# Optimization experiments

Measured on AMD Instinct MI355X. Metric: run time of the kernel, lower is better.

## Reference

```python
import jax, jax.numpy as jnp
import numpy as np

N_NODES = 100000
N_EDGES = 3200000
IN_CH = 128
OUT_CH = 64
HID = 2 * OUT_CH  # 128


def gcn_conv(x, W, b, src, dst, num_nodes):
    """PyG GCNConv: D^{-1/2}(A+I)D^{-1/2} X W + b (add_self_loops=True, normalize=True)."""
    h = x @ W  # [N, C_out]
    # degree on target nodes, edge weight 1, plus 1 for the self loop
    deg = jax.ops.segment_sum(jnp.ones_like(dst, dtype=h.dtype), dst, num_segments=num_nodes) + 1.0
    dinv = jax.lax.rsqrt(deg)  # deg >= 1 so no inf handling needed
    norm = dinv[src] * dinv[dst]  # [E]
    agg = jax.ops.segment_sum(h[src] * norm[:, None], dst, num_segments=num_nodes)
    agg = agg + h * (dinv * dinv)[:, None]  # self-loop contribution, norm = dinv_i^2
    return agg + b


def setup_inputs() -> dict:
    key = jax.random.key(0)
    ks = jax.random.split(key, 8)
    s_in = 1.0 / np.sqrt(IN_CH)
    s_hid = 1.0 / np.sqrt(HID)
    s_out = 1.0 / np.sqrt(OUT_CH)
    return {
        "x": jax.random.normal(ks[0], (N_NODES, IN_CH), dtype=jnp.float32),
        "edge_index": jax.random.randint(ks[1], (2, N_EDGES), 0, N_NODES, dtype=jnp.int64),
        "W1n": jax.random.normal(ks[2], (IN_CH, HID), dtype=jnp.float32) * s_in,
        "b1n": jnp.zeros((HID,), jnp.float32),
        "W2n": jax.random.normal(ks[3], (HID, OUT_CH), dtype=jnp.float32) * s_hid,
        "b2n": jnp.zeros((OUT_CH,), jnp.float32),
        "W1e": jax.random.normal(ks[4], (OUT_CH, HID), dtype=jnp.float32) * s_out,
        "b1e": jnp.zeros((HID,), jnp.float32),
        "W2e": jax.random.normal(ks[5], (HID, OUT_CH), dtype=jnp.float32) * s_hid,
        "b2e": jnp.zeros((OUT_CH,), jnp.float32),
    }


def reference(x, edge_index, W1n, b1n, W2n, b2n, W1e, b1e, W2e, b2e):
    src, dst = edge_index[0], edge_index[1]
    n = x.shape[0]
    h = jax.nn.relu(gcn_conv(x, W1n, b1n, src, dst, n))
    mu = gcn_conv(h, W2n, b2n, src, dst, n)
    e = jax.nn.relu(gcn_conv(mu, W1e, b1e, src, dst, n))
    logstd = gcn_conv(e, W2e, b2e, src, dst, n)
    return (mu, logstd)
```

## Files before the change

kernel.cpp:

```cpp
#include <hip/hip_runtime.h>
#include <hip/hip_bf16.h>


typedef unsigned int uint;
typedef unsigned short ushort_t;
typedef __attribute__((ext_vector_type(8))) short bf16x8;
typedef __attribute__((ext_vector_type(4))) float f32x4;

__device__ __forceinline__ float bflo(uint u) { return __uint_as_float(u << 16); }
__device__ __forceinline__ float bfhi(uint u) { return __uint_as_float(u & 0xFFFF0000u); }
__device__ __forceinline__ ushort_t f2bf(float f) {
  union { float f; uint u; } v; v.f = f;
  uint r = v.u + 0x7FFFu + ((v.u >> 16) & 1u);
  return (ushort_t)(r >> 16);
}

#define BSH 4
#define SCAP 128
#define BFCAP 1024


__global__ void k_scatter(const int* __restrict__ src, const int* __restrict__ dst,
                          int E, int* __restrict__ cnt, uint* __restrict__ ebuf) {
  int i = blockIdx.x * 256 + threadIdx.x;
  const int sub = blockIdx.x & 7;
  if (2 * i + 1 < E) {
    int2 s2 = *(const int2*)(src + 2 * i);
    int2 d2 = *(const int2*)(dst + 2 * i);
    int c0 = ((d2.x >> BSH) << 3) + sub;
    int p0 = atomicAdd(&cnt[c0], 1);
    if (p0 < SCAP) ebuf[c0 * SCAP + p0] = (uint)s2.x | ((uint)(d2.x & 15) << 17);
    int c1 = ((d2.y >> BSH) << 3) + sub;
    int p1 = atomicAdd(&cnt[c1], 1);
    if (p1 < SCAP) ebuf[c1 * SCAP + p1] = (uint)s2.y | ((uint)(d2.y & 15) << 17);
  }
}

__global__ __launch_bounds__(1024) void k_bscan(const int* __restrict__ cnt,
                                                int* __restrict__ boffs,
                                                int NBK, int E) {
  __shared__ int sc[1024];
  const int t = threadIdx.x;
  int run = 0;
  for (int base = 0; base < NBK; base += 1024) {
    int i = base + t;
    int c = 0;
    if (i < NBK) {
      const int4* q = (const int4*)(cnt + i * 8);
      int4 a = q[0], b = q[1];
      c = a.x + a.y + a.z + a.w + b.x + b.y + b.z + b.w;
    }
    sc[t] = c;
    __syncthreads();
    for (int off = 1; off < 1024; off <<= 1) {
      int u = (t >= off) ? sc[t - off] : 0;
      __syncthreads();
      sc[t] += u;
      __syncthreads();
    }
    if (i < NBK) boffs[i] = run + sc[t] - c;
    int total = sc[1023];
    __syncthreads();
    run += total;
  }
  if (t == 0) boffs[NBK] = E;
}

__global__ __launch_bounds__(256) void k_binfill(const int* __restrict__ cnt,
                                                 const int* __restrict__ boffs,
                                                 const uint* __restrict__ ebuf,
                                                 int* __restrict__ csr,
                                                 int* __restrict__ offs,
                                                 float* __restrict__ dinv,
                                                 int N, int E) {
  __shared__ uint led[BFCAP];
  __shared__ int lcnt[16], lbase[16], lpre[9];
  const int b = blockIdx.x;
  const int t = threadIdx.x;
  if (t < 16) lcnt[t] = 0;
  if (t == 0) {
    int r = 0;
#pragma unroll
    for (int s = 0; s < 8; s++) {
      lpre[s] = r;
      int c = cnt[b * 8 + s];
      r += (c < SCAP ? c : SCAP);
    }
    lpre[8] = r;
  }
  __syncthreads();
#pragma unroll
  for (int s = 0; s < 8; s++) {
    int base = lpre[s], len = lpre[s + 1] - base;
    for (int e = t; e < len; e += 256) led[base + e] = ebuf[(b * 8 + s) * SCAP + e];
  }
  const int total = lpre[8];
  __syncthreads();
  for (int e = t; e < total; e += 256) atomicAdd(&lcnt[(led[e] >> 17) & 15], 1);
  __syncthreads();
  if (t == 0) {
    int run = boffs[b];
#pragma unroll
    for (int k = 0; k < 16; k++) { lbase[k] = run; run += lcnt[k]; }
  }
  __syncthreads();
  if (t < 16) {
    int node = (b << BSH) + t;
    if (node < N) {
      offs[node] = lbase[t];
      dinv[node] = rsqrtf((float)(lcnt[t] + 1));
    }
  }
  if (b == 0 && t == 16) offs[N] = E;
  if (t < 16) lcnt[t] = 0;
  __syncthreads();
  for (int e = t; e < total; e += 256) {
    uint p = led[e];
    int k = (int)((p >> 17) & 15);
    int r = atomicAdd(&lcnt[k], 1);
    csr[lbase[k] + r] = (int)(p & 0x1FFFF);
  }
}


__global__ void k_cvt(const float* __restrict__ in, uint* __restrict__ out, int n8) {
  int i = blockIdx.x * 256 + threadIdx.x;
  if (i < n8) {
    float4 a = *(const float4*)(in + 8 * i);
    float4 b = *(const float4*)(in + 8 * i + 4);
    uint4 o;
    o.x = (uint)f2bf(a.x) | ((uint)f2bf(a.y) << 16);
    o.y = (uint)f2bf(a.z) | ((uint)f2bf(a.w) << 16);
    o.z = (uint)f2bf(b.x) | ((uint)f2bf(b.y) << 16);
    o.w = (uint)f2bf(b.z) | ((uint)f2bf(b.w) << 16);
    *(uint4*)(out + 4 * i) = o;
  }
}


template <int CIN, int COUT>
__global__ __launch_bounds__(256) void k_mgemm(const __hip_bfloat16* __restrict__ X,
                                               const float* __restrict__ W,
                                               const float* __restrict__ dinv,
                                               __hip_bfloat16* __restrict__ H, int N) {
  constexpr int KCH = CIN / 32;
  constexpr int TPW = COUT / 64;
  const int wid = threadIdx.x >> 6, lane = threadIdx.x & 63;
  const int l16 = lane & 15, lg = lane >> 4;
  const int cb = wid * (COUT / 4);
  bf16x8 bfr[TPW][KCH];
#pragma unroll
  for (int t = 0; t < TPW; t++) {
#pragma unroll
    for (int ch = 0; ch < KCH; ch++) {
      const int col = cb + t * 16 + l16;
      const int k0 = ch * 32 + lg * 8;
#pragma unroll
      for (int j = 0; j < 8; j++)
        bfr[t][ch][j] = (short)f2bf(W[(size_t)(k0 + j) * COUT + col]);
    }
  }
  const int RB = (N + 15) >> 4;
  for (int rb = blockIdx.x; rb < RB; rb += gridDim.x) {
    const int r0 = rb << 4;
    const int arow = min(r0 + l16, N - 1);
    const __hip_bfloat16* xr = X + (size_t)arow * CIN + lg * 8;
    bf16x8 afr[KCH];
#pragma unroll
    for (int ch = 0; ch < KCH; ch++) afr[ch] = *(const bf16x8*)(xr + ch * 32);
    f32x4 acc[TPW];
#pragma unroll
    for (int t = 0; t < TPW; t++) acc[t] = (f32x4){0.f, 0.f, 0.f, 0.f};
#pragma unroll
    for (int ch = 0; ch < KCH; ch++) {
#pragma unroll
      for (int t = 0; t < TPW; t++)
        acc[t] = __builtin_amdgcn_mfma_f32_16x16x32_bf16(afr[ch], bfr[t][ch], acc[t], 0, 0, 0);
    }
#pragma unroll
    for (int r = 0; r < 4; r++) {
      const int orow = r0 + lg * 4 + r;
      if (orow < N) {
        const float dv = dinv[orow];
#pragma unroll
        for (int t = 0; t < TPW; t++)
          *(ushort_t*)(H + (size_t)orow * COUT + cb + t * 16 + l16) = f2bf(dv * acc[t][r]);
      }
    }
  }
}


__global__ __launch_bounds__(256) void k_agg128(const __hip_bfloat16* __restrict__ H,
                                                const int* __restrict__ offs,
                                                const int* __restrict__ csr,
                                                const float* __restrict__ dinv,
                                                const float* __restrict__ b,
                                                __hip_bfloat16* __restrict__ OUT, int N) {
  const int lane = threadIdx.x & 63, wid = threadIdx.x >> 6;
  const int i = blockIdx.x * 4 + wid;
  if (i >= N) return;
  const int c = lane * 2;
  const float b0 = b[c], b1 = b[c + 1];
  const int beg = offs[i], end = offs[i + 1];
  float a0 = 0, a1 = 0;
  int e = beg;
  for (; e + 4 <= end; e += 4) {
    int s0 = csr[e], s1 = csr[e + 1], s2 = csr[e + 2], s3 = csr[e + 3];
    uint h0 = *(const uint*)(H + (size_t)s0 * 128 + c);
    uint h1 = *(const uint*)(H + (size_t)s1 * 128 + c);
    uint h2 = *(const uint*)(H + (size_t)s2 * 128 + c);
    uint h3 = *(const uint*)(H + (size_t)s3 * 128 + c);
    a0 += bflo(h0) + bflo(h1) + bflo(h2) + bflo(h3);
    a1 += bfhi(h0) + bfhi(h1) + bfhi(h2) + bfhi(h3);
  }
  for (; e < end; e++) {
    int s = csr[e];
    uint h = *(const uint*)(H + (size_t)s * 128 + c);
    a0 += bflo(h);
    a1 += bfhi(h);
  }
  const float di = dinv[i];
  uint hs = *(const uint*)(H + (size_t)i * 128 + c);
  float r0 = di * (a0 + bflo(hs)) + b0;
  float r1 = di * (a1 + bfhi(hs)) + b1;
  r0 = fmaxf(r0, 0.f);
  r1 = fmaxf(r1, 0.f);
  *(uint*)(OUT + (size_t)i * 128 + c) = (uint)f2bf(r0) | ((uint)f2bf(r1) << 16);
}


__global__ __launch_bounds__(256) void k_agg64(const __hip_bfloat16* __restrict__ H,
                                               const int* __restrict__ offs,
                                               const int* __restrict__ csr,
                                               const float* __restrict__ dinv,
                                               const float* __restrict__ b,
                                               float* __restrict__ OUT,
                                               __hip_bfloat16* __restrict__ MIR, int N) {
  const int lane = threadIdx.x & 63, wid = threadIdx.x >> 6;
  const int i = blockIdx.x * 4 + wid;
  if (i >= N) return;
  const int half = lane >> 5;
  const int c = (lane & 31) * 2;
  const float b0 = b[c], b1 = b[c + 1];
  const int beg = offs[i], end = offs[i + 1];
  float a0 = 0, a1 = 0;
  int e = beg + half;
  for (; e + 6 < end; e += 8) {
    int s0 = csr[e], s1 = csr[e + 2], s2 = csr[e + 4], s3 = csr[e + 6];
    uint h0 = *(const uint*)(H + (size_t)s0 * 64 + c);
    uint h1 = *(const uint*)(H + (size_t)s1 * 64 + c);
    uint h2 = *(const uint*)(H + (size_t)s2 * 64 + c);
    uint h3 = *(const uint*)(H + (size_t)s3 * 64 + c);
    a0 += bflo(h0) + bflo(h1) + bflo(h2) + bflo(h3);
    a1 += bfhi(h0) + bfhi(h1) + bfhi(h2) + bfhi(h3);
  }
  for (; e < end; e += 2) {
    int s = csr[e];
    uint h = *(const uint*)(H + (size_t)s * 64 + c);
    a0 += bflo(h);
    a1 += bfhi(h);
  }
  a0 += __shfl_xor(a0, 32);
  a1 += __shfl_xor(a1, 32);
  const float di = dinv[i];
  uint hs = *(const uint*)(H + (size_t)i * 64 + c);
  float r0 = di * (a0 + bflo(hs)) + b0;
  float r1 = di * (a1 + bfhi(hs)) + b1;
  if (lane < 32) {
    *(float2*)(OUT + (size_t)i * 64 + c) = make_float2(r0, r1);
    if (MIR) *(uint*)(MIR + (size_t)i * 64 + c) = (uint)f2bf(r0) | ((uint)f2bf(r1) << 16);
  }
}


extern "C" void kernel_launch(void* const* d_in, const int* in_sizes, int n_in,
                              void* d_out, int out_size, void* d_ws, size_t ws_size,
                              hipStream_t stream) {
  const float* x   = (const float*)d_in[0];
  const int*   ei  = (const int*)d_in[1];
  const float* W1n = (const float*)d_in[2];
  const float* b1n = (const float*)d_in[3];
  const float* W2n = (const float*)d_in[4];
  const float* b2n = (const float*)d_in[5];
  const float* W1e = (const float*)d_in[6];
  const float* b1e = (const float*)d_in[7];
  const float* W2e = (const float*)d_in[8];
  const float* b2e = (const float*)d_in[9];
  float* out = (float*)d_out;

  const int N = in_sizes[0] / 128;
  const int E = in_sizes[1] / 2;
  const int NBK = (N + 15) >> BSH;
  const int* src = ei;
  const int* dst = ei + E;

  char* p = (char*)d_ws;
  auto alloc = [&](size_t bytes) {
    void* q = (void*)p;
    p += (bytes + 255) & ~(size_t)255;
    return q;
  };
  int*   cnt   = (int*)alloc((size_t)NBK * 8 * 4);
  int*   boffs = (int*)alloc((size_t)(NBK + 1) * 4);
  int*   offs  = (int*)alloc((size_t)(N + 1) * 4);
  float* dinv  = (float*)alloc((size_t)N * 4);
  int*   csr   = (int*)alloc((size_t)E * 4);
  __hip_bfloat16* hbuf = (__hip_bfloat16*)alloc((size_t)N * 128 * 2);
  __hip_bfloat16* abuf = (__hip_bfloat16*)alloc((size_t)N * 128 * 2);
  uint* ebuf = (uint*)hbuf;

  const int RB = (N + 15) >> 4;
  const int GEMM_GRID = RB < 1024 ? RB : 1024;

  hipMemsetAsync(cnt, 0, (size_t)NBK * 8 * 4, stream);
  k_scatter<<<(E / 2 + 255) / 256, 256, 0, stream>>>(src, dst, E, cnt, ebuf);
  k_bscan<<<1, 1024, 0, stream>>>(cnt, boffs, NBK, E);
  k_binfill<<<NBK, 256, 0, stream>>>(cnt, boffs, ebuf, csr, offs, dinv, N, E);

  k_cvt<<<(N * 128 / 8 + 255) / 256, 256, 0, stream>>>(x, (uint*)abuf, N * 128 / 8);

  k_mgemm<128, 128><<<GEMM_GRID, 256, 0, stream>>>(abuf, W1n, dinv, hbuf, N);
  k_agg128<<<(N + 3) / 4, 256, 0, stream>>>(hbuf, offs, csr, dinv, b1n, abuf, N);

  k_mgemm<128, 64><<<GEMM_GRID, 256, 0, stream>>>(abuf, W2n, dinv, hbuf, N);
  k_agg64<<<(N + 3) / 4, 256, 0, stream>>>(hbuf, offs, csr, dinv, b2n, out, abuf, N);

  k_mgemm<64, 128><<<GEMM_GRID, 256, 0, stream>>>(abuf, W1e, dinv, hbuf, N);
  k_agg128<<<(N + 3) / 4, 256, 0, stream>>>(hbuf, offs, csr, dinv, b1e, abuf, N);

  k_mgemm<128, 64><<<GEMM_GRID, 256, 0, stream>>>(abuf, W2e, dinv, hbuf, N);
  k_agg64<<<(N + 3) / 4, 256, 0, stream>>>(hbuf, offs, csr, dinv, b2e, out + (size_t)N * 64,
                                           (__hip_bfloat16*)nullptr, N);
}
```

Before: 766.6 us.

## Slice aggregation by 16-column feature chunks with persistent grid; XCC-based scatter sub-bucket

The aggregation kernels now run on a fixed persistent grid. Each wave processes a 16-column slice of the feature matrix for every node before moving to the next slice, with 8 edges handled in parallel per wave and shuffle reductions. The goal is to shrink the gather working set per pass (32 B per row) so that the randomly accessed H slice fits in cache across the edge gather. The cost is 8 or 4 passes over the CSR indices and narrow 4-byte gathers. The scatter kernel also picks its sub-bucket from the hardware XCC id register instead of the block index, which lowers cross-die atomic contention.

After: 1.573 ms. +105.2%, slower.

```diff
diff --git a/kernel.cpp b/kernel.cpp
--- a/kernel.cpp
+++ b/kernel.cpp
@@ -18,12 +18,15 @@
 #define BSH 4
 #define SCAP 128
 #define BFCAP 1024
+#define AGG_GRID 2048
+
+#define XCC_HWREG 6164
 
 
 __global__ void k_scatter(const int* __restrict__ src, const int* __restrict__ dst,
                           int E, int* __restrict__ cnt, uint* __restrict__ ebuf) {
   int i = blockIdx.x * 256 + threadIdx.x;
-  const int sub = blockIdx.x & 7;
+  const int sub = __builtin_amdgcn_s_getreg(XCC_HWREG) & 7;
   if (2 * i + 1 < E) {
     int2 s2 = *(const int2*)(src + 2 * i);
     int2 d2 = *(const int2*)(dst + 2 * i);
@@ -197,38 +200,48 @@
                                                 const float* __restrict__ dinv,
                                                 const float* __restrict__ b,
                                                 __hip_bfloat16* __restrict__ OUT, int N) {
-  const int lane = threadIdx.x & 63, wid = threadIdx.x >> 6;
-  const int i = blockIdx.x * 4 + wid;
-  if (i >= N) return;
-  const int c = lane * 2;
-  const float b0 = b[c], b1 = b[c + 1];
-  const int beg = offs[i], end = offs[i + 1];
-  float a0 = 0, a1 = 0;
-  int e = beg;
-  for (; e + 4 <= end; e += 4) {
-    int s0 = csr[e], s1 = csr[e + 1], s2 = csr[e + 2], s3 = csr[e + 3];
-    uint h0 = *(const uint*)(H + (size_t)s0 * 128 + c);
-    uint h1 = *(const uint*)(H + (size_t)s1 * 128 + c);
-    uint h2 = *(const uint*)(H + (size_t)s2 * 128 + c);
-    uint h3 = *(const uint*)(H + (size_t)s3 * 128 + c);
-    a0 += bflo(h0) + bflo(h1) + bflo(h2) + bflo(h3);
-    a1 += bfhi(h0) + bfhi(h1) + bfhi(h2) + bfhi(h3);
-  }
-  for (; e < end; e++) {
-    int s = csr[e];
-    uint h = *(const uint*)(H + (size_t)s * 128 + c);
-    a0 += bflo(h);
-    a1 += bfhi(h);
-  }
-  const float di = dinv[i];
-  uint hs = *(const uint*)(H + (size_t)i * 128 + c);
-  float r0 = di * (a0 + bflo(hs)) + b0;
-  float r1 = di * (a1 + bfhi(hs)) + b1;
-  r0 = fmaxf(r0, 0.f);
-  r1 = fmaxf(r1, 0.f);
-  *(uint*)(OUT + (size_t)i * 128 + c) = (uint)f2bf(r0) | ((uint)f2bf(r1) << 16);
-}
-
+  const int lane = threadIdx.x & 63;
+  const int gw = (blockIdx.x * 256 + threadIdx.x) >> 6;
+  const int TW = AGG_GRID * 4;
+  const int ep = lane >> 3;
+  const int c = (lane & 7) * 2;
+#pragma unroll 1
+  for (int s = 0; s < 8; s++) {
+    const int cbase = s * 16 + c;
+    const float b0 = b[cbase], b1 = b[cbase + 1];
+    const __hip_bfloat16* Hs = H + cbase;
+    for (int i = gw; i < N; i += TW) {
+      const int beg = offs[i], end = offs[i + 1];
+      float a0 = 0, a1 = 0;
+      int e = beg + ep;
+      for (; e + 8 < end; e += 16) {
+        int s0 = csr[e], s1 = csr[e + 8];
+        uint h0 = *(const uint*)(Hs + (size_t)s0 * 128);
+        uint h1 = *(const uint*)(Hs + (size_t)s1 * 128);
+        a0 += bflo(h0) + bflo(h1);
+        a1 += bfhi(h0) + bfhi(h1);
+      }
+      if (e < end) {
+        int s0 = csr[e];
+        uint h0 = *(const uint*)(Hs + (size_t)s0 * 128);
+        a0 += bflo(h0);
+        a1 += bfhi(h0);
+      }
+      a0 += __shfl_xor(a0, 8);  a1 += __shfl_xor(a1, 8);
+      a0 += __shfl_xor(a0, 16); a1 += __shfl_xor(a1, 16);
+      a0 += __shfl_xor(a0, 32); a1 += __shfl_xor(a1, 32);
+      if (ep == 0) {
+        const float di = dinv[i];
+        uint hs = *(const uint*)(Hs + (size_t)i * 128);
+        float r0 = di * (a0 + bflo(hs)) + b0;
+        float r1 = di * (a1 + bfhi(hs)) + b1;
+        r0 = fmaxf(r0, 0.f);
+        r1 = fmaxf(r1, 0.f);
+        *(uint*)(OUT + (size_t)i * 128 + cbase) = (uint)f2bf(r0) | ((uint)f2bf(r1) << 16);
+      }
+    }
+  }
+}
 
 __global__ __launch_bounds__(256) void k_agg64(const __hip_bfloat16* __restrict__ H,
                                                const int* __restrict__ offs,
@@ -237,39 +250,45 @@
                                                const float* __restrict__ b,
                                                float* __restrict__ OUT,
                                                __hip_bfloat16* __restrict__ MIR, int N) {
-  const int lane = threadIdx.x & 63, wid = threadIdx.x >> 6;
-  const int i = blockIdx.x * 4 + wid;
-  if (i >= N) return;
-  const int half = lane >> 5;
-  const int c = (lane & 31) * 2;
-  const float b0 = b[c], b1 = b[c + 1];
-  const int beg = offs[i], end = offs[i + 1];
-  float a0 = 0, a1 = 0;
-  int e = beg + half;
-  for (; e + 6 < end; e += 8) {
-    int s0 = csr[e], s1 = csr[e + 2], s2 = csr[e + 4], s3 = csr[e + 6];
-    uint h0 = *(const uint*)(H + (size_t)s0 * 64 + c);
-    uint h1 = *(const uint*)(H + (size_t)s1 * 64 + c);
-    uint h2 = *(const uint*)(H + (size_t)s2 * 64 + c);
-    uint h3 = *(const uint*)(H + (size_t)s3 * 64 + c);
-    a0 += bflo(h0) + bflo(h1) + bflo(h2) + bflo(h3);
-    a1 += bfhi(h0) + bfhi(h1) + bfhi(h2) + bfhi(h3);
-  }
-  for (; e < end; e += 2) {
-    int s = csr[e];
-    uint h = *(const uint*)(H + (size_t)s * 64 + c);
-    a0 += bflo(h);
-    a1 += bfhi(h);
-  }
-  a0 += __shfl_xor(a0, 32);
-  a1 += __shfl_xor(a1, 32);
-  const float di = dinv[i];
-  uint hs = *(const uint*)(H + (size_t)i * 64 + c);
-  float r0 = di * (a0 + bflo(hs)) + b0;
-  float r1 = di * (a1 + bfhi(hs)) + b1;
-  if (lane < 32) {
-    *(float2*)(OUT + (size_t)i * 64 + c) = make_float2(r0, r1);
-    if (MIR) *(uint*)(MIR + (size_t)i * 64 + c) = (uint)f2bf(r0) | ((uint)f2bf(r1) << 16);
+  const int lane = threadIdx.x & 63;
+  const int gw = (blockIdx.x * 256 + threadIdx.x) >> 6;
+  const int TW = AGG_GRID * 4;
+  const int ep = lane >> 3;
+  const int c = (lane & 7) * 2;
+#pragma unroll 1
+  for (int s = 0; s < 4; s++) {
+    const int cbase = s * 16 + c;
+    const float b0 = b[cbase], b1 = b[cbase + 1];
+    const __hip_bfloat16* Hs = H + cbase;
+    for (int i = gw; i < N; i += TW) {
+      const int beg = offs[i], end = offs[i + 1];
+      float a0 = 0, a1 = 0;
+      int e = beg + ep;
+      for (; e + 8 < end; e += 16) {
+        int s0 = csr[e], s1 = csr[e + 8];
+        uint h0 = *(const uint*)(Hs + (size_t)s0 * 64);
+        uint h1 = *(const uint*)(Hs + (size_t)s1 * 64);
+        a0 += bflo(h0) + bflo(h1);
+        a1 += bfhi(h0) + bfhi(h1);
+      }
+      if (e < end) {
+        int s0 = csr[e];
+        uint h0 = *(const uint*)(Hs + (size_t)s0 * 64);
+        a0 += bflo(h0);
+        a1 += bfhi(h0);
+      }
+      a0 += __shfl_xor(a0, 8);  a1 += __shfl_xor(a1, 8);
+      a0 += __shfl_xor(a0, 16); a1 += __shfl_xor(a1, 16);
+      a0 += __shfl_xor(a0, 32); a1 += __shfl_xor(a1, 32);
+      if (ep == 0) {
+        const float di = dinv[i];
+        uint hs = *(const uint*)(Hs + (size_t)i * 64);
+        float r0 = di * (a0 + bflo(hs)) + b0;
+        float r1 = di * (a1 + bfhi(hs)) + b1;
+        *(float2*)(OUT + (size_t)i * 64 + cbase) = make_float2(r0, r1);
+        if (MIR) *(uint*)(MIR + (size_t)i * 64 + cbase) = (uint)f2bf(r0) | ((uint)f2bf(r1) << 16);
+      }
+    }
   }
 }
 
@@ -321,15 +340,15 @@
   k_cvt<<<(N * 128 / 8 + 255) / 256, 256, 0, stream>>>(x, (uint*)abuf, N * 128 / 8);
 
   k_mgemm<128, 128><<<GEMM_GRID, 256, 0, stream>>>(abuf, W1n, dinv, hbuf, N);
-  k_agg128<<<(N + 3) / 4, 256, 0, stream>>>(hbuf, offs, csr, dinv, b1n, abuf, N);
+  k_agg128<<<AGG_GRID, 256, 0, stream>>>(hbuf, offs, csr, dinv, b1n, abuf, N);
 
   k_mgemm<128, 64><<<GEMM_GRID, 256, 0, stream>>>(abuf, W2n, dinv, hbuf, N);
-  k_agg64<<<(N + 3) / 4, 256, 0, stream>>>(hbuf, offs, csr, dinv, b2n, out, abuf, N);
+  k_agg64<<<AGG_GRID, 256, 0, stream>>>(hbuf, offs, csr, dinv, b2n, out, abuf, N);
 
   k_mgemm<64, 128><<<GEMM_GRID, 256, 0, stream>>>(abuf, W1e, dinv, hbuf, N);
-  k_agg128<<<(N + 3) / 4, 256, 0, stream>>>(hbuf, offs, csr, dinv, b1e, abuf, N);
+  k_agg128<<<AGG_GRID, 256, 0, stream>>>(hbuf, offs, csr, dinv, b1e, abuf, N);
 
   k_mgemm<128, 64><<<GEMM_GRID, 256, 0, stream>>>(abuf, W2e, dinv, hbuf, N);
-  k_agg64<<<(N + 3) / 4, 256, 0, stream>>>(hbuf, offs, csr, dinv, b2e, out + (size_t)N * 64,
-                                           (__hip_bfloat16*)nullptr, N);
-}
+  k_agg64<<<AGG_GRID, 256, 0, stream>>>(hbuf, offs, csr, dinv, b2e, out + (size_t)N * 64,
+                                        (__hip_bfloat16*)nullptr, N);
+}
```
